# Performance work log

Hardware: AMD Instinct MI355X
Metric: run time of the kernel (lower is better)

Reference implementation:

```python
import jax, jax.numpy as jnp
import numpy as np


def setup_inputs() -> dict:
    key = jax.random.key(0)
    k1, k2 = jax.random.split(key)
    pred_feat = jax.random.normal(k1, (20000, 3), dtype=jnp.float32)
    gt_feat = jax.random.normal(k2, (20000, 4), dtype=jnp.float32)
    return {"pred_feat": pred_feat, "gt_feat": gt_feat}


def reference(pred_feat, gt_feat):
    # pred: [N,3], gt xyz: [M,3]
    pred = pred_feat                      # [N,3]
    gt = gt_feat[:, :3]                   # [M,3]
    # squared pairwise distances via ||p||^2 + ||g||^2 - 2 p.g  -> [N, M]
    p2 = jnp.sum(pred * pred, axis=-1, keepdims=True)          # [N,1]
    g2 = jnp.sum(gt * gt, axis=-1, keepdims=True).T             # [1,M]
    d2 = p2 + g2 - 2.0 * jnp.einsum('nd,md->nm', pred, gt)      # [N,M]
    d2 = jnp.maximum(d2, 0.0)
    # bidirectional chamfer with mean point reduction
    fwd = jnp.mean(jnp.min(d2, axis=1))   # pred -> gt
    bwd = jnp.mean(jnp.min(d2, axis=0))   # gt -> pred
    return fwd + bwd
```

## Files before the change

kernel.cpp:

```cpp
#include <hip/hip_runtime.h>

typedef __bf16 bf16x8 __attribute__((ext_vector_type(8)));
typedef float f32x16 __attribute__((ext_vector_type(16)));

#define BLK      256
#define WPB      4
#define TPW      2
#define TPB      (WPB * TPW)
#define CH_TILES 20
#define CH_SLOTS (CH_TILES * 32)

__device__ __forceinline__ float min3f(float a, float b, float c) {
    float d;
    asm("v_min3_f32 %0, %1, %2, %3" : "=v"(d) : "v"(a), "v"(b), "v"(c));
    return d;
}
__device__ __forceinline__ f32x16 mfma_tile(bf16x8 a, bf16x8 b, f32x16 zc) {
    f32x16 d;
    asm("v_mfma_f32_32x32x16_bf16 %0, %1, %2, %3"
        : "=&v"(d) : "v"(a), "v"(b), "v"(zc));
    return d;
}
__device__ __forceinline__ void fold8(float& r0, float& r1, float& r2, float& r3,
                                      float& r4, float& r5, float& r6, float& r7,
                                      f32x16 d) {
    asm("s_nop 7\n\t"
        "s_nop 7\n\t"
        "s_nop 7\n\t"
        "s_nop 7\n\t"
        "v_min3_f32 %0, %8,  %9,  %0\n\t"
        "v_min3_f32 %1, %10, %11, %1\n\t"
        "v_min3_f32 %2, %12, %13, %2\n\t"
        "v_min3_f32 %3, %14, %15, %3\n\t"
        "v_min3_f32 %4, %16, %17, %4\n\t"
        "v_min3_f32 %5, %18, %19, %5\n\t"
        "v_min3_f32 %6, %20, %21, %6\n\t"
        "v_min3_f32 %7, %22, %23, %7"
        : "+v"(r0), "+v"(r1), "+v"(r2), "+v"(r3),
          "+v"(r4), "+v"(r5), "+v"(r6), "+v"(r7)
        : "v"(d[0]),  "v"(d[1]),  "v"(d[2]),  "v"(d[3]),
          "v"(d[4]),  "v"(d[5]),  "v"(d[6]),  "v"(d[7]),
          "v"(d[8]),  "v"(d[9]),  "v"(d[10]), "v"(d[11]),
          "v"(d[12]), "v"(d[13]), "v"(d[14]), "v"(d[15]));
}
#define FOLD(rm, dv) fold8(rm[0], rm[1], rm[2], rm[3], rm[4], rm[5], rm[6], rm[7], dv)

__device__ __forceinline__ unsigned int f2key(float f) {
    unsigned int b = __float_as_uint(f);
    return (b & 0x80000000u) ? ~b : (b | 0x80000000u);
}
__device__ __forceinline__ float key2f(unsigned int k) {
    unsigned int b = (k & 0x80000000u) ? (k ^ 0x80000000u) : ~k;
    return __uint_as_float(b);
}
__device__ __forceinline__ void splitp(float x, float y, float z,
    __bf16& xh, __bf16& xl, __bf16& yh, __bf16& yl,
    __bf16& zh, __bf16& zl, __bf16& s2h, __bf16& s2l)
{
    float s2 = fmaf(x, x, fmaf(y, y, z*z));
    xh = (__bf16)x;  xl = (__bf16)(x - (float)xh);
    yh = (__bf16)y;  yl = (__bf16)(y - (float)yh);
    zh = (__bf16)z;  zl = (__bf16)(z - (float)zh);
    s2h = (__bf16)s2; s2l = (__bf16)(s2 - (float)s2h);
}

__global__ __launch_bounds__(BLK, 4) void chamfer_mfma(
    const float* __restrict__ pred, const float* __restrict__ gt,
    unsigned int* __restrict__ minsAll, int nP, int nG)
{
    __shared__ bf16x8 sh[CH_TILES * 64];

    const int dir  = blockIdx.z;
    const int nOwn = dir ? nG : nP;
    const int nStr = dir ? nP : nG;
    const int ownTiles = (nOwn + 31) >> 5;
    unsigned int* mins = minsAll + (dir ? nP : 0);

    const int tid = threadIdx.x, wave = tid >> 6, lane = tid & 63, col = lane & 31;
    const __bf16 one = (__bf16)1.0f, zero = (__bf16)0.0f, big = (__bf16)1.0e30f;

    #pragma unroll
    for (int j = tid; j < CH_SLOTS; j += BLK) {
        const int g = blockIdx.y * CH_SLOTS + j;
        float x = 0.f, y = 0.f, z = 0.f;
        const bool v = g < nStr;
        if (v) {
            if (dir == 0) { float4 G = ((const float4*)gt)[g]; x = G.x; y = G.y; z = G.z; }
            else          { x = pred[3*g]; y = pred[3*g+1]; z = pred[3*g+2]; }
        }
        __bf16 xh, xl, yh, yl, zh, zl, s2h, s2l;
        splitp(x, y, z, xh, xl, yh, yl, zh, zl, s2h, s2l);
        if (!v) { s2h = big; s2l = big; }
        const int t = j >> 5, q = j & 31;
        sh[t*64 + q]      = bf16x8{one, one, s2h, s2l, xh, xl, xh, yh};
        sh[t*64 + 32 + q] = bf16x8{yl, yh, zh, zl, zh, zero, zero, zero};
    }

    const int tileA = blockIdx.x * TPB + wave * TPW;
    const int tileB = tileA + 1;
    bf16x8 bf0, bf1;
    {
        auto mk = [&](int tile) -> bf16x8 {
            int i = tile * 32 + col; i = min(i, nOwn - 1);
            float x, y, z;
            if (dir == 0) { x = pred[3*i]; y = pred[3*i+1]; z = pred[3*i+2]; }
            else          { float4 G = ((const float4*)gt)[i]; x = G.x; y = G.y; z = G.z; }
            __bf16 xh, xl, yh, yl, zh, zl, q2h, q2l;
            splitp(x, y, z, xh, xl, yh, yl, zh, zl, q2h, q2l);
            const __bf16 m2xh = (__bf16)(-2.f*(float)xh), m2xl = (__bf16)(-2.f*(float)xl);
            const __bf16 m2yh = (__bf16)(-2.f*(float)yh), m2yl = (__bf16)(-2.f*(float)yl);
            const __bf16 m2zh = (__bf16)(-2.f*(float)zh), m2zl = (__bf16)(-2.f*(float)zl);
            return (lane < 32)
                ? bf16x8{q2h, q2l, one, one, m2xh, m2xh, m2xl, m2yh}
                : bf16x8{m2yh, m2yl, m2zh, m2zh, m2zl, zero, zero, zero};
        };
        bf0 = mk(tileA);
        bf1 = mk(tileB);
    }
    __syncthreads();

    float rm0[8], rm1[8];
    #pragma unroll
    for (int j = 0; j < 8; ++j) { rm0[j] = 3.0e38f; rm1[j] = 3.0e38f; }
    f32x16 zc = {};

    bf16x8 aA = sh[lane];
    f32x16 d00 = mfma_tile(aA, bf0, zc);
    f32x16 d01 = mfma_tile(aA, bf1, zc);
    bf16x8 aB = sh[64 + lane];
    f32x16 d10 = mfma_tile(aB, bf0, zc);
    f32x16 d11 = mfma_tile(aB, bf1, zc);

    #pragma unroll
    for (int t = 2; t < CH_TILES; t += 2) {
        bf16x8 a0 = sh[t*64 + lane];
        FOLD(rm0, d00); FOLD(rm1, d01);
        d00 = mfma_tile(a0, bf0, zc);
        d01 = mfma_tile(a0, bf1, zc);
        bf16x8 a1 = sh[(t+1)*64 + lane];
        FOLD(rm0, d10); FOLD(rm1, d11);
        d10 = mfma_tile(a1, bf0, zc);
        d11 = mfma_tile(a1, bf1, zc);
    }
    FOLD(rm0, d00); FOLD(rm1, d01);
    FOLD(rm0, d10); FOLD(rm1, d11);

    float mA, mB;
    { float a = min3f(rm0[0], rm0[1], rm0[2]);
      float b = min3f(rm0[3], rm0[4], rm0[5]);
      float c = min3f(rm0[6], rm0[7], a);
      mA = fminf(fminf(b, c), 3.0e38f); }
    { float a = min3f(rm1[0], rm1[1], rm1[2]);
      float b = min3f(rm1[3], rm1[4], rm1[5]);
      float c = min3f(rm1[6], rm1[7], a);
      mB = fminf(fminf(b, c), 3.0e38f); }

    const int idxA = tileA * 32 + col;
    const int idxB = tileB * 32 + col;
    if (tileA < ownTiles && idxA < nOwn) atomicMin(&mins[idxA], f2key(mA));
    if (tileB < ownTiles && idxB < nOwn) atomicMin(&mins[idxB], f2key(mB));
}

__global__ __launch_bounds__(BLK) void chamfer_reduce1(
    const unsigned int* __restrict__ mins, float* __restrict__ part,
    int nP, int nG, float invP, float invG)
{
    const int i = blockIdx.x * BLK + threadIdx.x;
    float v = 0.f;
    if (i < nP + nG) {
        const unsigned int k = mins[i];
        const float d = (k == 0xFFFFFFFFu) ? 1.0e30f : fmaxf(0.f, key2f(k));
        v = d * (i < nP ? invP : invG);
    }
    #pragma unroll
    for (int o = 32; o > 0; o >>= 1) v += __shfl_xor(v, o);
    __shared__ float r[WPB];
    const int wid = threadIdx.x >> 6, lane = threadIdx.x & 63;
    if (lane == 0) r[wid] = v;
    __syncthreads();
    if (threadIdx.x == 0) part[blockIdx.x] = r[0] + r[1] + r[2] + r[3];
}

__global__ __launch_bounds__(BLK) void chamfer_reduce2(
    const float* __restrict__ part, float* __restrict__ out, int nPart)
{
    float v = 0.f;
    for (int i = threadIdx.x; i < nPart; i += BLK) v += part[i];
    #pragma unroll
    for (int o = 32; o > 0; o >>= 1) v += __shfl_xor(v, o);
    __shared__ float r[WPB];
    const int wid = threadIdx.x >> 6, lane = threadIdx.x & 63;
    if (lane == 0) r[wid] = v;
    __syncthreads();
    if (threadIdx.x == 0) out[0] = r[0] + r[1] + r[2] + r[3];
}

extern "C" void kernel_launch(void* const* d_in, const int* in_sizes, int n_in,
                              void* d_out, int out_size, void* d_ws, size_t ws_size,
                              hipStream_t stream)
{
    const float* pred = (const float*)d_in[0];
    const float* gt   = (const float*)d_in[1];
    const int nP = in_sizes[0] / 3;
    const int nG = in_sizes[1] / 4;
    const int nTot = nP + nG;

    unsigned int* mins = (unsigned int*)d_ws;
    const int nPart = (nTot + BLK - 1) / BLK;
    float* part = (float*)((char*)d_ws + (((size_t)nTot * 4 + 255) & ~(size_t)255));
    (void)ws_size; (void)n_in; (void)out_size;

    hipMemsetAsync(mins, 0xFF, (size_t)nTot * 4, stream);

    const int maxN = nP > nG ? nP : nG;
    const int tilesMax = (maxN + 31) / 32;
    dim3 grid((tilesMax + TPB - 1) / TPB,
              (maxN + CH_SLOTS - 1) / CH_SLOTS,
              2);
    chamfer_mfma<<<grid, BLK, 0, stream>>>(pred, gt, mins, nP, nG);

    chamfer_reduce1<<<nPart, BLK, 0, stream>>>(mins, part, nP, nG,
                                               1.0f / (float)nP, 1.0f / (float)nG);
    chamfer_reduce2<<<1, BLK, 0, stream>>>(part, (float*)d_out, nPart);
}
```

Measured before the change: 44.96 us.

## Precompute split bf16 point fragments in a pre-pass and stream from global

Adds a pre-pass kernel that converts both point sets once into padded hi/lo bf16 records with squared norms. The main MFMA kernel then loads these records straight from global memory instead of rebuilding them into shared memory per block. That removes the LDS staging and the __syncthreads, and each block now covers 40 streamed tiles (SPLIT=16) instead of 20, giving fewer blocks and fewer atomics. The cost is an extra kernel launch, extra global traffic through L2, and s_nop padding before each MFMA. The padded size is fixed at 20480 points, so larger inputs would break.

Result: slower. 76.74 us (+70.7%).

```diff
diff --git a/kernel.cpp b/kernel.cpp
--- a/kernel.cpp
+++ b/kernel.cpp
@@ -7,8 +7,10 @@
 #define WPB      4
 #define TPW      2
 #define TPB      (WPB * TPW)
-#define CH_TILES 20
-#define CH_SLOTS (CH_TILES * 32)
+#define SPLIT    16
+#define TPS      40
+#define PAD_TILES (SPLIT * TPS)
+#define PAD_SLOTS (PAD_TILES * 32)
 
 __device__ __forceinline__ float min3f(float a, float b, float c) {
     float d;
@@ -17,7 +19,8 @@
 }
 __device__ __forceinline__ f32x16 mfma_tile(bf16x8 a, bf16x8 b, f32x16 zc) {
     f32x16 d;
-    asm("v_mfma_f32_32x32x16_bf16 %0, %1, %2, %3"
+    asm("s_nop 3\n\t"
+        "v_mfma_f32_32x32x16_bf16 %0, %1, %2, %3"
         : "=&v"(d) : "v"(a), "v"(b), "v"(zc));
     return d;
 }
@@ -64,37 +67,65 @@
     s2h = (__bf16)s2; s2l = (__bf16)(s2 - (float)s2h);
 }
 
+__device__ __forceinline__ bf16x8 mk_afrag(uint4 r, bool hi) {
+    uint4 h;
+    if (!hi) {
+        h.x = 0x3F803F80u;
+        h.y = r.w;
+        h.z = r.x;
+        h.w = (r.x & 0xFFFFu) | (r.y << 16);
+    } else {
+        h.x = (r.y >> 16) | (r.y << 16);
+        h.y = r.z;
+        h.z = r.z & 0xFFFFu;
+        h.w = 0u;
+    }
+    return __builtin_bit_cast(bf16x8, h);
+}
+
+__global__ void expandSplit(const float* __restrict__ pred, const float* __restrict__ gt,
+                            bf16x8* __restrict__ predS, bf16x8* __restrict__ gtS,
+                            int nP, int nG)
+{
+    const int i = blockIdx.x * blockDim.x + threadIdx.x;
+    if (i >= PAD_SLOTS) return;
+    const __bf16 zero = (__bf16)0.0f, big = (__bf16)1.0e30f;
+    {
+        bf16x8 h = {zero, zero, zero, zero, zero, zero, big, big};
+        if (i < nP) {
+            float x = pred[3*i], y = pred[3*i+1], z = pred[3*i+2];
+            __bf16 xh, xl, yh, yl, zh, zl, s2h, s2l;
+            splitp(x, y, z, xh, xl, yh, yl, zh, zl, s2h, s2l);
+            h = bf16x8{xh, xl, yh, yl, zh, zl, s2h, s2l};
+        }
+        predS[i] = h;
+    }
+    {
+        bf16x8 h = {zero, zero, zero, zero, zero, zero, big, big};
+        if (i < nG) {
+            float4 G = ((const float4*)gt)[i];
+            __bf16 xh, xl, yh, yl, zh, zl, s2h, s2l;
+            splitp(G.x, G.y, G.z, xh, xl, yh, yl, zh, zl, s2h, s2l);
+            h = bf16x8{xh, xl, yh, yl, zh, zl, s2h, s2l};
+        }
+        gtS[i] = h;
+    }
+}
+
 __global__ __launch_bounds__(BLK, 4) void chamfer_mfma(
     const float* __restrict__ pred, const float* __restrict__ gt,
+    const bf16x8* __restrict__ predS, const bf16x8* __restrict__ gtS,
     unsigned int* __restrict__ minsAll, int nP, int nG)
 {
-    __shared__ bf16x8 sh[CH_TILES * 64];
-
     const int dir  = blockIdx.z;
     const int nOwn = dir ? nG : nP;
-    const int nStr = dir ? nP : nG;
     const int ownTiles = (nOwn + 31) >> 5;
+    const uint4* __restrict__ strR = (const uint4*)(dir ? predS : gtS);
     unsigned int* mins = minsAll + (dir ? nP : 0);
 
     const int tid = threadIdx.x, wave = tid >> 6, lane = tid & 63, col = lane & 31;
-    const __bf16 one = (__bf16)1.0f, zero = (__bf16)0.0f, big = (__bf16)1.0e30f;
-
-    #pragma unroll
-    for (int j = tid; j < CH_SLOTS; j += BLK) {
-        const int g = blockIdx.y * CH_SLOTS + j;
-        float x = 0.f, y = 0.f, z = 0.f;
-        const bool v = g < nStr;
-        if (v) {
-            if (dir == 0) { float4 G = ((const float4*)gt)[g]; x = G.x; y = G.y; z = G.z; }
-            else          { x = pred[3*g]; y = pred[3*g+1]; z = pred[3*g+2]; }
-        }
-        __bf16 xh, xl, yh, yl, zh, zl, s2h, s2l;
-        splitp(x, y, z, xh, xl, yh, yl, zh, zl, s2h, s2l);
-        if (!v) { s2h = big; s2l = big; }
-        const int t = j >> 5, q = j & 31;
-        sh[t*64 + q]      = bf16x8{one, one, s2h, s2l, xh, xl, xh, yh};
-        sh[t*64 + 32 + q] = bf16x8{yl, yh, zh, zl, zh, zero, zero, zero};
-    }
+    const bool hi = lane >= 32;
+    const __bf16 one = (__bf16)1.0f, zero = (__bf16)0.0f;
 
     const int tileA = blockIdx.x * TPB + wave * TPW;
     const int tileB = tileA + 1;
@@ -117,28 +148,33 @@
         bf0 = mk(tileA);
         bf1 = mk(tileB);
     }
-    __syncthreads();
 
     float rm0[8], rm1[8];
     #pragma unroll
     for (int j = 0; j < 8; ++j) { rm0[j] = 3.0e38f; rm1[j] = 3.0e38f; }
     f32x16 zc = {};
 
-    bf16x8 aA = sh[lane];
+    const int t0 = blockIdx.y * TPS;
+
+    uint4 rA = strR[(t0 + 0) * 32 + col];
+    uint4 rB = strR[(t0 + 1) * 32 + col];
+    bf16x8 aA = mk_afrag(rA, hi);
     f32x16 d00 = mfma_tile(aA, bf0, zc);
     f32x16 d01 = mfma_tile(aA, bf1, zc);
-    bf16x8 aB = sh[64 + lane];
+    bf16x8 aB = mk_afrag(rB, hi);
     f32x16 d10 = mfma_tile(aB, bf0, zc);
     f32x16 d11 = mfma_tile(aB, bf1, zc);
 
     #pragma unroll
-    for (int t = 2; t < CH_TILES; t += 2) {
-        bf16x8 a0 = sh[t*64 + lane];
+    for (int t = 2; t < TPS; t += 2) {
+        uint4 r0 = strR[(t0 + t) * 32 + col];
+        uint4 r1 = strR[(t0 + t + 1) * 32 + col];
         FOLD(rm0, d00); FOLD(rm1, d01);
+        bf16x8 a0 = mk_afrag(r0, hi);
         d00 = mfma_tile(a0, bf0, zc);
         d01 = mfma_tile(a0, bf1, zc);
-        bf16x8 a1 = sh[(t+1)*64 + lane];
         FOLD(rm0, d10); FOLD(rm1, d11);
+        bf16x8 a1 = mk_afrag(r1, hi);
         d10 = mfma_tile(a1, bf0, zc);
         d11 = mfma_tile(a1, bf1, zc);
     }
@@ -205,20 +241,31 @@
     const int nG = in_sizes[1] / 4;
     const int nTot = nP + nG;
 
-    unsigned int* mins = (unsigned int*)d_ws;
-    const int nPart = (nTot + BLK - 1) / BLK;
-    float* part = (float*)((char*)d_ws + (((size_t)nTot * 4 + 255) & ~(size_t)255));
+    char* ws = (char*)d_ws;
+    size_t off = 0;
+    auto take = [&](size_t bytes) -> void* {
+        void* p = ws + off;
+        off = (off + bytes + 255) & ~(size_t)255;
+        return p;
+    };
+    bf16x8* predS = (bf16x8*)take((size_t)PAD_SLOTS * 16);
+    bf16x8* gtS   = (bf16x8*)take((size_t)PAD_SLOTS * 16);
+    unsigned int* mins = (unsigned int*)take((size_t)nTot * 4);
+    float* part = (float*)predS;
     (void)ws_size; (void)n_in; (void)out_size;
 
     hipMemsetAsync(mins, 0xFF, (size_t)nTot * 4, stream);
+
+    expandSplit<<<(PAD_SLOTS + 255) / 256, 256, 0, stream>>>(pred, gt, predS, gtS, nP, nG);
 
     const int maxN = nP > nG ? nP : nG;
     const int tilesMax = (maxN + 31) / 32;
     dim3 grid((tilesMax + TPB - 1) / TPB,
-              (maxN + CH_SLOTS - 1) / CH_SLOTS,
+              SPLIT,
               2);
-    chamfer_mfma<<<grid, BLK, 0, stream>>>(pred, gt, mins, nP, nG);
-
+    chamfer_mfma<<<grid, BLK, 0, stream>>>(pred, gt, predS, gtS, mins, nP, nG);
+
+    const int nPart = (nTot + BLK - 1) / BLK;
     chamfer_reduce1<<<nPart, BLK, 0, stream>>>(mins, part, nP, nG,
                                                1.0f / (float)nP, 1.0f / (float)nG);
     chamfer_reduce2<<<1, BLK, 0, stream>>>(part, (float*)d_out, nPart);
```
